# Performance work log

Hardware: AMD Instinct MI355X
Metric: run time of the kernel (lower is better)

Reference implementation:

```python
import jax, jax.numpy as jnp
from jax import lax
import numpy as np

B, T = 64, 256
V, E = 50000, 128
U1, U2, U3, U4 = 256, 256, 512, 5000


def lstm_scan(x, W, U, b, reverse=False):
    """Keras-style LSTM, gate order i,f,g,o; activation=relu, recurrent_activation=sigmoid.
    x: [B, T, D]. Returns (hs [B, T, H], h_last [B, H]). With reverse=True the
    sequence is processed back-to-front and outputs are stacked in original
    time order (matching Keras Bidirectional's go_backwards + re-reverse)."""
    Bn = x.shape[0]
    H = U.shape[0]
    h0 = jnp.zeros((Bn, H), dtype=x.dtype)
    c0 = jnp.zeros((Bn, H), dtype=x.dtype)

    def step(carry, xt):
        h, c = carry
        z = xt @ W + h @ U + b  # [B, 4H]
        i, f, g, o = jnp.split(z, 4, axis=-1)
        i = jax.nn.sigmoid(i)
        f = jax.nn.sigmoid(f)
        o = jax.nn.sigmoid(o)
        c = f * c + i * jax.nn.relu(g)
        h = o * jax.nn.relu(c)
        return (h, c), h

    xs = jnp.swapaxes(x, 0, 1)  # [T, B, D]
    (h_last, _), hs = lax.scan(step, (h0, c0), xs, reverse=reverse)
    return jnp.swapaxes(hs, 0, 1), h_last


def setup_inputs() -> dict:
    key = jax.random.key(0)
    ks = jax.random.split(key, 16)
    s = 0.05

    def n(k, shape):
        return jax.random.normal(k, shape, dtype=jnp.float32) * s

    tokens = jax.random.randint(ks[0], (B, T), 0, V, dtype=jnp.int32)
    emb = n(ks[1], (V, E))
    # BiLSTM forward / backward direction weights
    W1f, U1f, b1f = n(ks[2], (E, 4 * U1)), n(ks[3], (U1, 4 * U1)), jnp.zeros((4 * U1,), jnp.float32)
    W1b, U1b, b1b = n(ks[4], (E, 4 * U1)), n(ks[5], (U1, 4 * U1)), jnp.zeros((4 * U1,), jnp.float32)
    # second LSTM (input = concat of both directions = 2*U1)
    W2, U2m, b2 = n(ks[6], (2 * U1, 4 * U2)), n(ks[7], (U2, 4 * U2)), jnp.zeros((4 * U2,), jnp.float32)
    # dense head
    W3, b3 = n(ks[8], (U2, U3)), jnp.zeros((U3,), jnp.float32)
    W4, b4 = n(ks[9], (U3, U4)), jnp.zeros((U4,), jnp.float32)
    return dict(tokens=tokens, emb=emb, W1f=W1f, U1f=U1f, b1f=b1f,
                W1b=W1b, U1b=U1b, b1b=b1b, W2=W2, U2m=U2m, b2=b2,
                W3=W3, b3=b3, W4=W4, b4=b4)


def reference(tokens, emb, W1f, U1f, b1f, W1b, U1b, b1b, W2, U2m, b2, W3, b3, W4, b4):
    # Inference path (training=False): all dropouts are identity.
    x = emb[tokens]                                 # [B, T, E]
    hs_f, _ = lstm_scan(x, W1f, U1f, b1f, reverse=False)
    hs_b, _ = lstm_scan(x, W1b, U1b, b1b, reverse=True)
    x = jnp.concatenate([hs_f, hs_b], axis=-1)      # [B, T, 2*U1]
    _, h = lstm_scan(x, W2, U2m, b2)                # [B, U2] (return_sequences=False)
    h = jax.nn.relu(h @ W3 + b3)                    # [B, U3]
    return jax.nn.softmax(h @ W4 + b4, axis=-1)     # [B, U4]
```

## Files before the change

kernel.cpp:

```cpp
#include <hip/hip_runtime.h>


typedef float v4f __attribute__((ext_vector_type(4)));
typedef short bs8 __attribute__((ext_vector_type(8)));
typedef int v8i __attribute__((ext_vector_type(8)));

#define BQ 64
#define TQ 256

__device__ __forceinline__ unsigned short f2bf(float f) {
  unsigned u = __builtin_bit_cast(unsigned, f);
  unsigned r = (u + 0x7FFFu + ((u >> 16) & 1u)) >> 16;
  return (unsigned short)r;
}
__device__ __forceinline__ unsigned char f2fp8(float v) {
  int p = __builtin_amdgcn_cvt_pk_fp8_f32(v, v, 0, false);
  return (unsigned char)(p & 0xff);
}
__device__ __forceinline__ v4f sigp(v4f a) {
  const float C1 = 9.765625e-4f;
  const float C3 = -1.24176353e-9f;
  const float C5 = 1.89478063e-15f;
  v4f r;
#pragma unroll
  for (int i = 0; i < 4; ++i) {
    float x = a[i];
    float y = x * x;
    float p = fmaf(y, C5, C3);
    p = fmaf(y, p, C1);
    r[i] = fmaf(x, p, 0.5f);
  }
  return r;
}
__device__ __forceinline__ v4f vmax0(v4f a) {
  v4f r;
#pragma unroll
  for (int i = 0; i < 4; ++i) r[i] = fmaxf(a[i], 0.f);
  return r;
}
__device__ __forceinline__ unsigned permb(unsigned hi, unsigned lo, unsigned sel) {
  unsigned d;
  asm("v_perm_b32 %0, %1, %2, %3" : "=v"(d) : "v"(hi), "v"(lo), "s"(sel));
  return d;
}
#define SCAN_BARRIER() asm volatile("s_waitcnt lgkmcnt(0)\n\ts_barrier" ::: "memory")

template <int LAYER, int KTOT>
__global__ __launch_bounds__(256, 2) void gemm_pack(
    const int* __restrict__ tokens, const float* __restrict__ emb,
    const unsigned short* __restrict__ hsA,
    const float* __restrict__ Bmat0, const float* __restrict__ Bmat1,
    const float* __restrict__ bias0, const float* __restrict__ bias1,
    unsigned short* __restrict__ xwp_out) {
  const int mblk = blockIdx.x, nblk = blockIdx.y, dir = blockIdx.z;
  const float* Bm = dir ? Bmat1 : Bmat0;
  const float* bi = dir ? bias1 : bias0;
  __shared__ unsigned short Abuf[128][72];
  __shared__ unsigned short Bbuf[128][72];
  const int tid = threadIdx.x;
  const int w = tid >> 6, lane = tid & 63, q = lane >> 4, l15 = lane & 15;

  v4f acc[8][2];
#pragma unroll
  for (int mt = 0; mt < 8; ++mt) {
    acc[mt][0] = (v4f)0.f;
    acc[mt][1] = (v4f)0.f;
  }

  for (int kc = 0; kc < KTOT / 64; ++kc) {
    {
      const int m = tid >> 1, hf = tid & 1;
      const long mg = (long)mblk * 128 + m;
      if (LAYER == 1) {
        const int t = (int)(mg >> 6), b = (int)(mg & 63);
        const int tok = tokens[b * TQ + t];
        const float* src = emb + (long)tok * 128 + kc * 64 + hf * 32;
#pragma unroll
        for (int i = 0; i < 32; i += 4) {
          float4 v = *(const float4*)(src + i);
          uint2 uu;
          uu.x = (unsigned)f2bf(v.x) | ((unsigned)f2bf(v.y) << 16);
          uu.y = (unsigned)f2bf(v.z) | ((unsigned)f2bf(v.w) << 16);
          *(uint2*)&Abuf[m][hf * 32 + i] = uu;
        }
      } else {
        const uint4* src = (const uint4*)(hsA + mg * 512 + kc * 64 + hf * 32);
#pragma unroll
        for (int i = 0; i < 4; ++i) *(uint4*)&Abuf[m][hf * 32 + i * 8] = src[i];
      }
    }
    {
      const int nn = tid & 127, kk0 = (tid >> 7) * 32;
      const float* bp = Bm + (long)(kc * 64 + kk0) * 1024 + nblk * 128 + nn;
#pragma unroll
      for (int i = 0; i < 32; i += 2) {
        float w0 = bp[(long)i * 1024];
        float w1 = bp[(long)(i + 1) * 1024];
        unsigned u = (unsigned)f2bf(w0) | ((unsigned)f2bf(w1) << 16);
        *(unsigned*)&Bbuf[nn][kk0 + i] = u;
      }
    }
    __syncthreads();
#pragma unroll
    for (int kf = 0; kf < 2; ++kf) {
      bs8 bfr[2];
#pragma unroll
      for (int ntl = 0; ntl < 2; ++ntl)
        bfr[ntl] = *(const bs8*)&Bbuf[w * 32 + ntl * 16 + l15][kf * 32 + q * 8];
#pragma unroll
      for (int mt = 0; mt < 8; ++mt) {
        bs8 afr = *(const bs8*)&Abuf[mt * 16 + l15][kf * 32 + q * 8];
        acc[mt][0] = __builtin_amdgcn_mfma_f32_16x16x32_bf16(afr, bfr[0], acc[mt][0], 0, 0, 0);
        acc[mt][1] = __builtin_amdgcn_mfma_f32_16x16x32_bf16(afr, bfr[1], acc[mt][1], 0, 0, 0);
      }
    }
    __syncthreads();
  }
  unsigned long long* xw64 = (unsigned long long*)xwp_out;
#pragma unroll
  for (int ntl = 0; ntl < 2; ++ntl) {
    const int ng = nblk * 128 + w * 32 + ntl * 16 + l15;
    const float bv = bi[ng];
    const int g = ng >> 8, j = ng & 255;
    const int tile = (j >> 4) * 4 + g;
#pragma unroll
    for (int mt = 0; mt < 8; ++mt) {
      const int mg = mblk * 128 + mt * 16;
      const int t = mg >> 6, s = (mg & 63) >> 4;
      const long dirS = (LAYER == 1) ? (dir * 4 + s) : s;
      unsigned long long pk = 0;
#pragma unroll
      for (int r = 0; r < 4; ++r) {
        float z = 256.f * (acc[mt][ntl][r] + bv);
        pk |= ((unsigned long long)f2bf(z)) << (16 * r);
      }
      xw64[((dirS * 256 + t) * 64 + tile) * 64 + q * 16 + l15] = pk;
    }
  }
}

template <int LAYER>
__global__ __launch_bounds__(1024) void scan_kernel(
    const float* __restrict__ U0, const float* __restrict__ U1,
    const unsigned short* __restrict__ xwp,
    unsigned short* __restrict__ hs, float* __restrict__ hfin) {
  const int bid = blockIdx.x;
  const int dir = (LAYER == 1) ? (bid >> 2) : 0;
  const int s = (LAYER == 1) ? (bid & 3) : bid;
  const int dirS = (LAYER == 1) ? (dir * 4 + s) : s;
  const float* Um = dir ? U1 : U0;
  const int tid = threadIdx.x, w = tid >> 6, lane = tid & 63;
  const int q = lane >> 4, l15 = lane & 15;

  __shared__ __align__(16) unsigned char hl[2][4352];

  v8i uf[4][2];
#pragma unroll
  for (int g = 0; g < 4; ++g) {
    const int n = g * 256 + w * 16 + l15;
#pragma unroll
    for (int kc = 0; kc < 2; ++kc) {
      v8i fr;
#pragma unroll
      for (int d = 0; d < 8; ++d) {
        const int k = kc * 128 + q * 32 + d * 4;
        float v0 = Um[(k + 0) * 1024 + n] * 8.f;
        float v1 = Um[(k + 1) * 1024 + n] * 8.f;
        float v2 = Um[(k + 2) * 1024 + n] * 8.f;
        float v3 = Um[(k + 3) * 1024 + n] * 8.f;
        int dw = __builtin_amdgcn_cvt_pk_fp8_f32(v0, v1, 0, false);
        dw = __builtin_amdgcn_cvt_pk_fp8_f32(v2, v3, dw, true);
        fr[d] = dw;
      }
      uf[g][kc] = fr;
    }
  }
  {
    unsigned char* hp = &hl[0][0];
    for (int i = tid; i < 4352; i += 1024) hp[i] = 0;
  }
  v4f c = (v4f)0.f;
  unsigned hpk0 = 0, hpk1 = 0;
  const unsigned SEL = 0x07060302u;

  const int sgn = (LAYER == 1 && dir == 1) ? -1 : 1;
  const int t0 = (LAYER == 1 && dir == 1) ? (TQ - 1) : 0;

  const unsigned long long* xptr =
      (const unsigned long long*)xwp + ((long)(dirS * 256 + t0) * 64 + w * 4) * 64 + lane;
  unsigned long long xv[4];
#pragma unroll
  for (int fi = 0; fi < 4; ++fi) xv[fi] = xptr[fi * 64];

  unsigned short* hsp =
      (LAYER == 1)
          ? hs + ((long)t0 * 64 + s * 16 + q * 4) * 512 + dir * 256 + w * 16 + l15
          : nullptr;
  const long hs_adv = (long)sgn * 64 * 512;
  const long x_adv = (long)sgn * 4096;

  const int rd_off = l15 * 272 + q * 32;
  const int wr_off = (q * 4) * 272 + w * 16 + l15;

  __syncthreads();

  int p = 0;
  for (int step = 0; step < TQ; ++step) {
    const unsigned char* hrd = &hl[p][rd_off];
    v8i afr = *(const v8i*)(hrd);

    if (LAYER == 1 && step > 0) {
      hsp[0 * 512] = (unsigned short)hpk0;
      hsp[1 * 512] = (unsigned short)(hpk0 >> 16);
      hsp[2 * 512] = (unsigned short)hpk1;
      hsp[3 * 512] = (unsigned short)(hpk1 >> 16);
      hsp += hs_adv;
    }

    v4f acc[4];
#pragma unroll
    for (int fi = 0; fi < 4; ++fi) {
      const unsigned lo = (unsigned)xv[fi];
      const unsigned hi = (unsigned)(xv[fi] >> 32);
      v4f t4;
      t4[0] = __builtin_bit_cast(float, lo << 16);
      t4[1] = __builtin_bit_cast(float, lo & 0xffff0000u);
      t4[2] = __builtin_bit_cast(float, hi << 16);
      t4[3] = __builtin_bit_cast(float, hi & 0xffff0000u);
      acc[fi] = t4;
    }

    if (step + 1 < TQ) {
      xptr += x_adv;
#pragma unroll
      for (int fi = 0; fi < 4; ++fi) xv[fi] = xptr[fi * 64];
    }

#pragma unroll
    for (int g = 0; g < 4; ++g)
      acc[g] = __builtin_amdgcn_mfma_scale_f32_16x16x128_f8f6f4(
          afr, uf[g][0], acc[g], 0, 0, 0, 127, 0, 127);
    afr = *(const v8i*)(hrd + 128);
#pragma unroll
    for (int g = 0; g < 4; ++g)
      acc[g] = __builtin_amdgcn_mfma_scale_f32_16x16x128_f8f6f4(
          afr, uf[g][1], acc[g], 0, 0, 0, 127, 0, 127);

    const v4f ii = sigp(acc[0]);
    const v4f ff = sigp(acc[1]);
    const v4f gr = vmax0(acc[2]) * (1.f / 256.f);
    const v4f oo = sigp(acc[3]);
    v4f cc;
#pragma unroll
    for (int i = 0; i < 4; ++i) cc[i] = fmaf(ff[i], c[i], ii[i] * gr[i]);
    c = cc;
    const v4f hh = oo * vmax0(cc);

    unsigned char* hwp = &hl[1 - p][wr_off];
#pragma unroll
    for (int r = 0; r < 4; ++r) hwp[r * 272] = f2fp8(hh[r] * 32.f);

    if (LAYER == 1) {
      const unsigned u0 = __builtin_bit_cast(unsigned, hh[0]) + 0x8000u;
      const unsigned u1 = __builtin_bit_cast(unsigned, hh[1]) + 0x8000u;
      const unsigned u2 = __builtin_bit_cast(unsigned, hh[2]) + 0x8000u;
      const unsigned u3 = __builtin_bit_cast(unsigned, hh[3]) + 0x8000u;
      hpk0 = permb(u1, u0, SEL);
      hpk1 = permb(u3, u2, SEL);
    }
    if (LAYER == 2 && step == TQ - 1) {
#pragma unroll
      for (int r = 0; r < 4; ++r)
        hfin[(s * 16 + q * 4 + r) * 256 + w * 16 + l15] = hh[r];
    }

    SCAN_BARRIER();
    p ^= 1;
  }
  if (LAYER == 1) {
    hsp[0 * 512] = (unsigned short)hpk0;
    hsp[1 * 512] = (unsigned short)(hpk0 >> 16);
    hsp[2 * 512] = (unsigned short)hpk1;
    hsp[3 * 512] = (unsigned short)(hpk1 >> 16);
  }
}

__global__ __launch_bounds__(256) void dense1_k(const float* __restrict__ hfin,
                                                const float* __restrict__ W3,
                                                const float* __restrict__ b3,
                                                float* __restrict__ r1) {
  __shared__ float hbuf[256];
  const int b = blockIdx.x, tid = threadIdx.x;
  hbuf[tid] = hfin[b * 256 + tid];
  __syncthreads();
#pragma unroll
  for (int nb = 0; nb < 2; ++nb) {
    const int n = nb * 256 + tid;
    float a = b3[n];
#pragma unroll 8
    for (int k = 0; k < 256; ++k) a = fmaf(hbuf[k], W3[k * 512 + n], a);
    r1[b * 512 + n] = fmaxf(a, 0.f);
  }
}

__global__ __launch_bounds__(256) void logits_k(const float* __restrict__ r1,
                                                const float* __restrict__ W4,
                                                const float* __restrict__ b4,
                                                float* __restrict__ lg) {
  const int tid = threadIdx.x;
  const int n = blockIdx.x * 32 + (tid & 31);
  const int bg = tid >> 5;
  if (n >= 5000) return;
  float a[8];
  const float bb = b4[n];
#pragma unroll
  for (int i = 0; i < 8; ++i) a[i] = bb;
  const float* rb = r1 + bg * 8 * 512;
#pragma unroll 4
  for (int k = 0; k < 512; ++k) {
    const float wv = W4[(long)k * 5000 + n];
#pragma unroll
    for (int i = 0; i < 8; ++i) a[i] = fmaf(rb[i * 512 + k], wv, a[i]);
  }
#pragma unroll
  for (int i = 0; i < 8; ++i) lg[(long)(bg * 8 + i) * 5000 + n] = a[i];
}

__global__ __launch_bounds__(256) void softmax_k(float* __restrict__ lg,
                                                 float* __restrict__ out) {
  __shared__ float red[256];
  const int b = blockIdx.x, tid = threadIdx.x;
  float* row = lg + (long)b * 5000;
  float mx = -3.4e38f;
  for (int n = tid; n < 5000; n += 256) mx = fmaxf(mx, row[n]);
  red[tid] = mx;
  __syncthreads();
  for (int st = 128; st > 0; st >>= 1) {
    if (tid < st) red[tid] = fmaxf(red[tid], red[tid + st]);
    __syncthreads();
  }
  mx = red[0];
  __syncthreads();
  float sum = 0.f;
  for (int n = tid; n < 5000; n += 256) {
    float e = __builtin_amdgcn_exp2f((row[n] - mx) * 1.44269504f);
    row[n] = e;
    sum += e;
  }
  red[tid] = sum;
  __syncthreads();
  for (int st = 128; st > 0; st >>= 1) {
    if (tid < st) red[tid] += red[tid + st];
    __syncthreads();
  }
  const float inv = 1.f / red[0];
  for (int n = tid; n < 5000; n += 256) out[(long)b * 5000 + n] = row[n] * inv;
}

extern "C" void kernel_launch(void* const* d_in, const int* in_sizes, int n_in,
                              void* d_out, int out_size, void* d_ws,
                              size_t ws_size, hipStream_t stream) {
  (void)in_sizes; (void)n_in; (void)out_size; (void)ws_size;
  const int* tokens = (const int*)d_in[0];
  const float* emb = (const float*)d_in[1];
  const float* W1f = (const float*)d_in[2];
  const float* U1f = (const float*)d_in[3];
  const float* b1f = (const float*)d_in[4];
  const float* W1b = (const float*)d_in[5];
  const float* U1b = (const float*)d_in[6];
  const float* b1b = (const float*)d_in[7];
  const float* W2 = (const float*)d_in[8];
  const float* U2 = (const float*)d_in[9];
  const float* b2 = (const float*)d_in[10];
  const float* W3 = (const float*)d_in[11];
  const float* b3 = (const float*)d_in[12];
  const float* W4 = (const float*)d_in[13];
  const float* b4 = (const float*)d_in[14];

  char* ws = (char*)d_ws;
  unsigned short* xwp = (unsigned short*)ws;
  unsigned short* hs = (unsigned short*)(ws + 67108864L);
  float* hfin = (float*)(ws + 67108864L + 16777216L);
  float* r1 = (float*)(ws + 67108864L + 16777216L + 65536L);
  float* lg = (float*)(ws + 67108864L + 16777216L + 65536L + 131072L);

  gemm_pack<1, 128><<<dim3(128, 8, 2), 256, 0, stream>>>(
      tokens, emb, nullptr, W1f, W1b, b1f, b1b, xwp);
  scan_kernel<1><<<8, 1024, 0, stream>>>(U1f, U1b, xwp, hs, nullptr);
  gemm_pack<2, 512><<<dim3(128, 8, 1), 256, 0, stream>>>(
      nullptr, nullptr, hs, W2, W2, b2, b2, xwp);
  scan_kernel<2><<<4, 1024, 0, stream>>>(U2, U2, xwp, nullptr, hfin);
  dense1_k<<<64, 256, 0, stream>>>(hfin, W3, b3, r1);
  logits_k<<<157, 256, 0, stream>>>(r1, W4, b4, lg);
  softmax_k<<<64, 256, 0, stream>>>(lg, (float*)d_out);
}
```

Measured before the change: 917.7 us.

## Pre-convert embedding and weights to bf16, fold gate scaling, use hardware bf16 pack

Adds a prep kernel that converts the whole embedding table and the W1f/W1b/W2 weights to bf16 once per call, so the gemm kernels load bf16 directly instead of converting fp32 on the fly. The 1/256 scale on the g gate is folded into a separate input-gate sigmoid polynomial, and the bf16 pack of h now uses the v_cvt_pk_bf16_f32 instruction in place of manual add-and-permute. The trade-off is that converting the full 50000-row embedding costs extra memory traffic, because only 16K rows are actually gathered.

```diff
diff --git a/kernel.cpp b/kernel.cpp
--- a/kernel.cpp
+++ b/kernel.cpp
@@ -32,28 +32,63 @@
   }
   return r;
 }
+__device__ __forceinline__ v4f sigpi(v4f a) {
+  const float C1 = 3.81469727e-6f;
+  const float C3 = -4.85063879e-12f;
+  const float C5 = 7.40148683e-18f;
+  v4f r;
+#pragma unroll
+  for (int i = 0; i < 4; ++i) {
+    float x = a[i];
+    float y = x * x;
+    float p = fmaf(y, C5, C3);
+    p = fmaf(y, p, C1);
+    r[i] = fmaf(x, p, 1.953125e-3f);
+  }
+  return r;
+}
 __device__ __forceinline__ v4f vmax0(v4f a) {
   v4f r;
 #pragma unroll
   for (int i = 0; i < 4; ++i) r[i] = fmaxf(a[i], 0.f);
   return r;
 }
-__device__ __forceinline__ unsigned permb(unsigned hi, unsigned lo, unsigned sel) {
+__device__ __forceinline__ unsigned cvt_pk_bf16(float lo, float hi) {
   unsigned d;
-  asm("v_perm_b32 %0, %1, %2, %3" : "=v"(d) : "v"(hi), "v"(lo), "s"(sel));
+  asm("v_cvt_pk_bf16_f32 %0, %1, %2" : "=v"(d) : "v"(lo), "v"(hi));
   return d;
 }
 #define SCAN_BARRIER() asm volatile("s_waitcnt lgkmcnt(0)\n\ts_barrier" ::: "memory")
+
+__global__ __launch_bounds__(256) void prep_bf(
+    const float* __restrict__ emb, const float* __restrict__ W1f,
+    const float* __restrict__ W1b, const float* __restrict__ W2,
+    unsigned short* __restrict__ embbf, unsigned short* __restrict__ W1bf,
+    unsigned short* __restrict__ W2bf) {
+  const long idx = (long)blockIdx.x * 256 + threadIdx.x;
+  const float* src;
+  unsigned short* dst;
+  long off;
+  if (idx < 1600000L) { src = emb; dst = embbf; off = idx; }
+  else if (idx < 1632768L) { src = W1f; dst = W1bf; off = idx - 1600000L; }
+  else if (idx < 1665536L) { src = W1b; dst = W1bf + 131072; off = idx - 1632768L; }
+  else { src = W2; dst = W2bf; off = idx - 1665536L; }
+  const float4 v = ((const float4*)src)[off];
+  const unsigned long long pk =
+      (unsigned long long)f2bf(v.x) | ((unsigned long long)f2bf(v.y) << 16) |
+      ((unsigned long long)f2bf(v.z) << 32) | ((unsigned long long)f2bf(v.w) << 48);
+  ((unsigned long long*)dst)[off] = pk;
+}
 
 template <int LAYER, int KTOT>
 __global__ __launch_bounds__(256, 2) void gemm_pack(
-    const int* __restrict__ tokens, const float* __restrict__ emb,
+    const int* __restrict__ tokens, const unsigned short* __restrict__ embbf,
     const unsigned short* __restrict__ hsA,
-    const float* __restrict__ Bmat0, const float* __restrict__ Bmat1,
+    const unsigned short* __restrict__ Bbf0, const unsigned short* __restrict__ Bbf1,
     const float* __restrict__ bias0, const float* __restrict__ bias1,
     unsigned short* __restrict__ xwp_out) {
   const int mblk = blockIdx.x, nblk = blockIdx.y, dir = blockIdx.z;
-  const float* Bm = dir ? Bmat1 : Bmat0;
+  const unsigned short* Bm = dir ? Bbf1 : Bbf0;
   const float* bi = dir ? bias1 : bias0;
   __shared__ unsigned short Abuf[128][72];
   __shared__ unsigned short Bbuf[128][72];
@@ -71,32 +106,24 @@
     {
       const int m = tid >> 1, hf = tid & 1;
       const long mg = (long)mblk * 128 + m;
+      const unsigned short* src;
       if (LAYER == 1) {
         const int t = (int)(mg >> 6), b = (int)(mg & 63);
         const int tok = tokens[b * TQ + t];
-        const float* src = emb + (long)tok * 128 + kc * 64 + hf * 32;
-#pragma unroll
-        for (int i = 0; i < 32; i += 4) {
-          float4 v = *(const float4*)(src + i);
-          uint2 uu;
-          uu.x = (unsigned)f2bf(v.x) | ((unsigned)f2bf(v.y) << 16);
-          uu.y = (unsigned)f2bf(v.z) | ((unsigned)f2bf(v.w) << 16);
-          *(uint2*)&Abuf[m][hf * 32 + i] = uu;
-        }
+        src = embbf + (long)tok * 128 + kc * 64 + hf * 32;
       } else {
-        const uint4* src = (const uint4*)(hsA + mg * 512 + kc * 64 + hf * 32);
-#pragma unroll
-        for (int i = 0; i < 4; ++i) *(uint4*)&Abuf[m][hf * 32 + i * 8] = src[i];
+        src = hsA + mg * 512 + kc * 64 + hf * 32;
       }
+#pragma unroll
+      for (int i = 0; i < 4; ++i)
+        *(uint4*)&Abuf[m][hf * 32 + i * 8] = ((const uint4*)src)[i];
     }
     {
       const int nn = tid & 127, kk0 = (tid >> 7) * 32;
-      const float* bp = Bm + (long)(kc * 64 + kk0) * 1024 + nblk * 128 + nn;
+      const unsigned short* bp = Bm + (long)(kc * 64 + kk0) * 1024 + nblk * 128 + nn;
 #pragma unroll
       for (int i = 0; i < 32; i += 2) {
-        float w0 = bp[(long)i * 1024];
-        float w1 = bp[(long)(i + 1) * 1024];
-        unsigned u = (unsigned)f2bf(w0) | ((unsigned)f2bf(w1) << 16);
+        unsigned u = (unsigned)bp[(long)i * 1024] | ((unsigned)bp[(long)(i + 1) * 1024] << 16);
         *(unsigned*)&Bbuf[nn][kk0 + i] = u;
       }
     }
@@ -181,7 +208,6 @@
   }
   v4f c = (v4f)0.f;
   unsigned hpk0 = 0, hpk1 = 0;
-  const unsigned SEL = 0x07060302u;
 
   const int sgn = (LAYER == 1 && dir == 1) ? -1 : 1;
   const int t0 = (LAYER == 1 && dir == 1) ? (TQ - 1) : 0;
@@ -246,9 +272,9 @@
       acc[g] = __builtin_amdgcn_mfma_scale_f32_16x16x128_f8f6f4(
           afr, uf[g][1], acc[g], 0, 0, 0, 127, 0, 127);
 
-    const v4f ii = sigp(acc[0]);
+    const v4f ii = sigpi(acc[0]);
     const v4f ff = sigp(acc[1]);
-    const v4f gr = vmax0(acc[2]) * (1.f / 256.f);
+    const v4f gr = vmax0(acc[2]);
     const v4f oo = sigp(acc[3]);
     v4f cc;
 #pragma unroll
@@ -261,12 +287,8 @@
     for (int r = 0; r < 4; ++r) hwp[r * 272] = f2fp8(hh[r] * 32.f);
 
     if (LAYER == 1) {
-      const unsigned u0 = __builtin_bit_cast(unsigned, hh[0]) + 0x8000u;
-      const unsigned u1 = __builtin_bit_cast(unsigned, hh[1]) + 0x8000u;
-      const unsigned u2 = __builtin_bit_cast(unsigned, hh[2]) + 0x8000u;
-      const unsigned u3 = __builtin_bit_cast(unsigned, hh[3]) + 0x8000u;
-      hpk0 = permb(u1, u0, SEL);
-      hpk1 = permb(u3, u2, SEL);
+      hpk0 = cvt_pk_bf16(hh[0], hh[1]);
+      hpk1 = cvt_pk_bf16(hh[2], hh[3]);
     }
     if (LAYER == 2 && step == TQ - 1) {
 #pragma unroll
@@ -384,11 +406,16 @@
   float* r1 = (float*)(ws + 67108864L + 16777216L + 65536L);
   float* lg = (float*)(ws + 67108864L + 16777216L + 65536L + 131072L);
 
+  unsigned short* W1bf = hs;
+  unsigned short* embbf = hs + 262144;
+  unsigned short* W2bf = (unsigned short*)lg;
+
+  prep_bf<<<7018, 256, 0, stream>>>(emb, W1f, W1b, W2, embbf, W1bf, W2bf);
   gemm_pack<1, 128><<<dim3(128, 8, 2), 256, 0, stream>>>(
-      tokens, emb, nullptr, W1f, W1b, b1f, b1b, xwp);
+      tokens, embbf, nullptr, W1bf, W1bf + 131072, b1f, b1b, xwp);
   scan_kernel<1><<<8, 1024, 0, stream>>>(U1f, U1b, xwp, hs, nullptr);
   gemm_pack<2, 512><<<dim3(128, 8, 1), 256, 0, stream>>>(
-      nullptr, nullptr, hs, W2, W2, b2, b2, xwp);
+      nullptr, nullptr, hs, W2bf, W2bf, b2, b2, xwp);
   scan_kernel<2><<<4, 1024, 0, stream>>>(U2, U2, xwp, nullptr, hfin);
   dense1_k<<<64, 256, 0, stream>>>(hfin, W3, b3, r1);
   logits_k<<<157, 256, 0, stream>>>(r1, W4, b4, lg);
```

Result: no change. 923.7 us (+0.7%).
